# Optimization experiments

Measured on AMD Instinct MI355X. Metric: run time of the kernel, lower is better.

## Reference

```python
import jax, jax.numpy as jnp
import numpy as np

CANVAS = 28
MARGIN = 2
HALF = CANVAS / 2.0          # 14
SCALE = CANVAS / 2.0 - MARGIN  # 12
P = 2        # num_paths
SEG = 4      # final segments
T = 8        # curve samples per bezier segment
AA = 2       # 2x2 = 4 anti-alias subsamples per pixel


def _lin(x, w, b):
    return x @ w + b


def _render(cp, widths, alphas):
    """diffvg-style rasterizer.
    cp: [B,P,S,4,2] cubic bezier control points, widths/alphas: [B,P].
    Returns [B,1,H,W] image over white background (paths paint dark).
    """
    B = cp.shape[0]
    t = jnp.linspace(0.0, 1.0, T)
    mt = 1.0 - t
    basis = jnp.stack([mt**3, 3*mt**2*t, 3*mt*t**2, t**3], axis=1)  # [T,4]
    pts = jnp.einsum('tk,bpskd->bpstd', basis, cp)                   # [B,P,S,T,2]
    q = pts.reshape(B, P, SEG * T, 2)                                # polyline [B,P,M,2]

    # 2x2 subpixel sample grid over the canvas
    Nf = CANVAS * AA
    c = (jnp.arange(Nf, dtype=jnp.float32) + 0.5) / AA               # fine coords
    sy, sx = jnp.meshgrid(c, c, indexing='ij')
    s = jnp.stack([sx.ravel(), sy.ravel()], axis=-1)                 # [Ns,2] (x,y)

    # stroke coverage: distance from each sample to nearest curve sample
    qq = jnp.sum(q * q, axis=-1)                                     # [B,P,M]
    ss = jnp.sum(s * s, axis=-1)                                     # [Ns]
    cr = jnp.einsum('bpmd,nd->bpmn', q, s)                           # [B,P,M,Ns]
    d2 = jnp.maximum(qq[..., None] + ss - 2.0 * cr, 0.0)
    dist = jnp.sqrt(jnp.min(d2, axis=2))                             # [B,P,Ns]
    stroke = jnp.clip(widths[..., None] * 0.5 + 0.5 - dist, 0.0, 1.0)

    # fill coverage: even-odd crossing number on the closed polyline
    qn = jnp.roll(q, -1, axis=2)
    x0, y0 = q[..., 0], q[..., 1]
    x1, y1 = qn[..., 0], qn[..., 1]
    syf, sxf = s[:, 1], s[:, 0]
    crossing_band = (y0[..., None] > syf) != (y1[..., None] > syf)   # [B,P,M,Ns]
    te = (syf - y0[..., None]) / (y1[..., None] - y0[..., None] + 1e-8)
    xint = x0[..., None] + te * (x1 - x0)[..., None]
    ncross = jnp.sum((crossing_band & (sxf < xint)).astype(jnp.int32), axis=2)
    inside = (ncross % 2).astype(dist.dtype)                         # [B,P,Ns]

    cov = jnp.maximum(inside, stroke)
    img = jnp.prod(1.0 - alphas[..., None] * cov, axis=1)            # composite over paths, bg=1
    img = img.reshape(B, CANVAS, AA, CANVAS, AA).mean(axis=(2, 4))   # AA resolve
    return img[:, None]                                              # [B,1,H,W]


def setup_inputs() -> dict:
    key = jax.random.key(0)
    ks = jax.random.split(key, 16)
    def W(k, i, o):
        return jax.random.normal(k, (i, o), jnp.float32) / np.sqrt(i).astype(np.float32)
    B = 128
    return {
        'x': jax.random.uniform(ks[0], (B, 1, 28, 28), jnp.float32),
        'eps': jax.random.normal(ks[1], (B, 64), jnp.float32),
        'enc_w1': W(ks[2], 784, 256), 'enc_b1': jnp.zeros((256,), jnp.float32),
        'enc_w2': W(ks[3], 256, 256), 'enc_b2': jnp.zeros((256,), jnp.float32),
        'mu_w': W(ks[4], 256, 64), 'mu_b': jnp.zeros((64,), jnp.float32),
        'lv_w': W(ks[5], 256, 64), 'lv_b': jnp.zeros((64,), jnp.float32),
        'dec_w1': W(ks[6], 64, 512), 'dec_b1': jnp.zeros((512,), jnp.float32),
        'dec_w2': W(ks[7], 512, 512), 'dec_b2': jnp.zeros((512,), jnp.float32),
        'cp_w': W(ks[8], 512, 28), 'cp_b': jnp.zeros((28,), jnp.float32),
        'ref_w1': W(ks[9], 92, 512), 'ref_b1': jnp.zeros((512,), jnp.float32),
        'ref_w2': W(ks[10], 512, 52), 'ref_b2': jnp.zeros((52,), jnp.float32),
        'wd_w': W(ks[11], 512, 2), 'wd_b': jnp.zeros((2,), jnp.float32),
        'al_w': W(ks[12], 512, 2), 'al_b': jnp.zeros((2,), jnp.float32),
    }


def reference(x, eps, enc_w1, enc_b1, enc_w2, enc_b2, mu_w, mu_b, lv_w, lv_b,
              dec_w1, dec_b1, dec_w2, dec_b2, cp_w, cp_b,
              ref_w1, ref_b1, ref_w2, ref_b2, wd_w, wd_b, al_w, al_b):
    B = x.shape[0]
    # encoder
    h = jax.nn.leaky_relu(_lin(x.reshape(B, -1), enc_w1, enc_b1), 0.2)
    h = jax.nn.leaky_relu(_lin(h, enc_w2, enc_b2), 0.2)
    mu = _lin(h, mu_w, mu_b)
    logvar = _lin(h, lv_w, lv_b)
    z = mu + eps * jnp.exp(0.5 * logvar)
    # hierarchical decoder
    h2 = jax.nn.selu(_lin(jax.nn.selu(_lin(z, dec_w1, dec_b1)), dec_w2, dec_b2))
    coarse = jnp.tanh(_lin(h2, cp_w, cp_b)).reshape(B, P, 7, 2) * SCALE + HALF
    pts_norm = (coarse - HALF) / SCALE
    h_in = jnp.concatenate([z, pts_norm.reshape(B, -1)], axis=-1)
    refined = jnp.tanh(_lin(jax.nn.selu(_lin(h_in, ref_w1, ref_b1)), ref_w2, ref_b2))
    points = refined.reshape(B, P, 13, 2) * SCALE + HALF
    seg_idx = 3 * jnp.arange(SEG)[:, None] + jnp.arange(4)[None, :]  # [S,4]
    control_points = points[:, :, seg_idx, :]                         # [B,P,S,4,2]
    widths = jax.nn.sigmoid(_lin(h2, wd_w, wd_b)) * 2.0 + 1.0
    alphas = jax.nn.sigmoid(_lin(h2, al_w, al_b))
    rendered = 1.0 - _render(control_points, widths, alphas)          # white digit on black
    return (rendered, mu, logvar, control_points, widths, alphas)
```

## Files before the change

### kernel.cpp

```cpp
#include <hip/hip_runtime.h>
#include <math.h>


#define O_MU  100352
#define O_LV  108544
#define O_CP  116736
#define O_WD  124928
#define O_AL  125184

__device__ __forceinline__ float leaky(float x) {
    return x >= 0.0f ? x : 0.2f * x;
}
__device__ __forceinline__ float selu(float x) {
    const float scale = 1.0507009873554805f;
    const float alpha = 1.6732632423543772f;
    return x > 0.0f ? scale * x : scale * (alpha * expm1f(x));
}

__global__ __launch_bounds__(512)
void pipeline(const float* __restrict__ x, const float* __restrict__ eps,
              const float* __restrict__ enc_w1, const float* __restrict__ enc_b1,
              const float* __restrict__ enc_w2, const float* __restrict__ enc_b2,
              const float* __restrict__ mu_w, const float* __restrict__ mu_b,
              const float* __restrict__ lv_w, const float* __restrict__ lv_b,
              const float* __restrict__ dec_w1, const float* __restrict__ dec_b1,
              const float* __restrict__ dec_w2, const float* __restrict__ dec_b2,
              const float* __restrict__ cp_w, const float* __restrict__ cp_b,
              const float* __restrict__ ref_w1, const float* __restrict__ ref_b1,
              const float* __restrict__ ref_w2, const float* __restrict__ ref_b2,
              const float* __restrict__ wd_w, const float* __restrict__ wd_b,
              const float* __restrict__ al_w, const float* __restrict__ al_b,
              float* __restrict__ out) {
    __shared__ float sX[784];
    __shared__ float sPart[512];
    __shared__ float sH1[256];
    __shared__ float sHe[256];
    __shared__ float sML[128];
    __shared__ float sIn[96];
    __shared__ float sD1[512];
    __shared__ float sH2[512];
    __shared__ float sR1[512];
    __shared__ float sP[56];
    __shared__ float sQ[128];
    __shared__ float sWA[4];

    const int row = blockIdx.x;
    const int tid = threadIdx.x;

    for (int i = tid; i < 784; i += 512) sX[i] = x[row * 784 + i];
    __syncthreads();

    {
        const int j = tid & 255, g = tid >> 8;
        const int k0 = g * 392;
        float a0 = 0.f, a1 = 0.f, a2 = 0.f, a3 = 0.f;
        for (int i = 0; i < 392; i += 4) {
            a0 = fmaf(sX[k0 + i + 0], enc_w1[(k0 + i + 0) * 256 + j], a0);
            a1 = fmaf(sX[k0 + i + 1], enc_w1[(k0 + i + 1) * 256 + j], a1);
            a2 = fmaf(sX[k0 + i + 2], enc_w1[(k0 + i + 2) * 256 + j], a2);
            a3 = fmaf(sX[k0 + i + 3], enc_w1[(k0 + i + 3) * 256 + j], a3);
        }
        sPart[tid] = (a0 + a1) + (a2 + a3);
    }
    __syncthreads();
    if (tid < 256) sH1[tid] = leaky(enc_b1[tid] + sPart[tid] + sPart[256 + tid]);
    __syncthreads();

    {
        const int j = tid & 255, g = tid >> 8;
        const int k0 = g * 128;
        float a0 = 0.f, a1 = 0.f, a2 = 0.f, a3 = 0.f;
        for (int i = 0; i < 128; i += 4) {
            a0 = fmaf(sH1[k0 + i + 0], enc_w2[(k0 + i + 0) * 256 + j], a0);
            a1 = fmaf(sH1[k0 + i + 1], enc_w2[(k0 + i + 1) * 256 + j], a1);
            a2 = fmaf(sH1[k0 + i + 2], enc_w2[(k0 + i + 2) * 256 + j], a2);
            a3 = fmaf(sH1[k0 + i + 3], enc_w2[(k0 + i + 3) * 256 + j], a3);
        }
        sPart[tid] = (a0 + a1) + (a2 + a3);
    }
    __syncthreads();
    if (tid < 256) sHe[tid] = leaky(enc_b2[tid] + sPart[tid] + sPart[256 + tid]);
    __syncthreads();

    {
        const int o = tid >> 2, g = tid & 3;
        const int j = o & 63;
        const bool is_lv = o >= 64;
        const float* __restrict__ W = is_lv ? lv_w : mu_w;
        float acc = 0.f;
        for (int k = g; k < 256; k += 4) acc = fmaf(sHe[k], W[k * 64 + j], acc);
        acc += __shfl_xor(acc, 1);
        acc += __shfl_xor(acc, 2);
        if (g == 0) {
            acc += is_lv ? lv_b[j] : mu_b[j];
            out[(is_lv ? O_LV : O_MU) + row * 64 + j] = acc;
            sML[o] = acc;
        }
    }
    __syncthreads();
    if (tid < 64)
        sIn[tid] = fmaf(eps[row * 64 + tid], expf(0.5f * sML[64 + tid]), sML[tid]);
    __syncthreads();

    {
        float acc = dec_b1[tid];
        for (int k = 0; k < 64; k++) acc = fmaf(sIn[k], dec_w1[k * 512 + tid], acc);
        sD1[tid] = selu(acc);
    }
    __syncthreads();

    {
        float a0 = dec_b2[tid], a1 = 0.f, a2 = 0.f, a3 = 0.f;
        for (int k = 0; k < 512; k += 4) {
            a0 = fmaf(sD1[k + 0], dec_w2[(k + 0) * 512 + tid], a0);
            a1 = fmaf(sD1[k + 1], dec_w2[(k + 1) * 512 + tid], a1);
            a2 = fmaf(sD1[k + 2], dec_w2[(k + 2) * 512 + tid], a2);
            a3 = fmaf(sD1[k + 3], dec_w2[(k + 3) * 512 + tid], a3);
        }
        sH2[tid] = selu((a0 + a1) + (a2 + a3));
    }
    __syncthreads();

    {
        const int o = tid >> 4, g = tid & 15;
        const float* __restrict__ W;
        int ldw, col;
        if (o < 28)      { W = cp_w; ldw = 28; col = o; }
        else if (o < 30) { W = wd_w; ldw = 2;  col = o - 28; }
        else             { W = al_w; ldw = 2;  col = o - 30; }
        float acc = 0.f;
        for (int k = g; k < 512; k += 16) acc = fmaf(sH2[k], W[k * ldw + col], acc);
        acc += __shfl_xor(acc, 1);
        acc += __shfl_xor(acc, 2);
        acc += __shfl_xor(acc, 4);
        acc += __shfl_xor(acc, 8);
        if (g == 0) {
            if (o < 28) {
                sIn[64 + o] = tanhf(acc + cp_b[col]);
            } else if (o < 30) {
                float v = 1.f / (1.f + expf(-(acc + wd_b[col])));
                v = fmaf(v, 2.f, 1.f);
                out[O_WD + row * 2 + col] = v;
                sWA[col] = v;
            } else {
                float v = 1.f / (1.f + expf(-(acc + al_b[col])));
                out[O_AL + row * 2 + col] = v;
                sWA[2 + col] = v;
            }
        }
    }
    __syncthreads();

    {
        float acc = ref_b1[tid];
        for (int k = 0; k < 92; k++) acc = fmaf(sIn[k], ref_w1[k * 512 + tid], acc);
        sR1[tid] = selu(acc);
    }
    __syncthreads();

    {
        const int o = tid >> 3, g = tid & 7;
        float acc = 0.f;
        if (o < 52)
            for (int k = g; k < 512; k += 8) acc = fmaf(sR1[k], ref_w2[k * 52 + o], acc);
        acc += __shfl_xor(acc, 1);
        acc += __shfl_xor(acc, 2);
        acc += __shfl_xor(acc, 4);
        if (g == 0 && o < 52)
            sP[o] = fmaf(tanhf(acc + ref_b2[o]), 12.f, 14.f);
    }
    __syncthreads();

    if (tid < 64) {
        int idx = tid;
        int p = idx >> 5, rest = idx & 31;
        int s = rest >> 3, kk = (rest >> 1) & 3, d = idx & 1;
        out[O_CP + row * 64 + idx] = sP[p * 26 + (3 * s + kk) * 2 + d];
    }
    if (tid < 128) {
        int idx = tid;
        int p = idx >> 6, s = (idx >> 4) & 3, ti = (idx >> 1) & 7, d = idx & 1;
        float t = (float)ti / 7.0f;
        float mt = 1.0f - t;
        float c0 = mt * mt * mt;
        float c1 = 3.f * mt * mt * t;
        float c2 = 3.f * mt * t * t;
        float c3 = t * t * t;
        const float* base = sP + p * 26 + (3 * s) * 2 + d;
        sQ[idx] = c0 * base[0] + c1 * base[2] + c2 * base[4] + c3 * base[6];
    }
    __syncthreads();

    const float2* __restrict__ sQ2 = (const float2*)sQ;
    for (int u = tid; u < 3136; u += 512) {
        const int pixel = u >> 2;
        const int sub = u & 3;
        const int py = pixel / 28;
        const int px = pixel - py * 28;
        const float sy = ((float)(2 * py + (sub >> 1)) + 0.5f) * 0.5f;
        const float sx = ((float)(2 * px + (sub & 1)) + 0.5f) * 0.5f;
        float img = 1.0f;
#pragma unroll
        for (int p = 0; p < 2; p++) {
            float dmin2 = 1e30f;
            int cnt = 0;
            float2 cur = sQ2[p * 32];
            bool bp = cur.y > sy;
#pragma unroll
            for (int m = 0; m < 32; m++) {
                float2 nxt = sQ2[p * 32 + ((m + 1) & 31)];
                float dx = sx - cur.x;
                float dy = sy - cur.y;
                dmin2 = fminf(dmin2, fmaf(dx, dx, dy * dy));
                bool bn = nxt.y > sy;
                float den = nxt.y - cur.y + 1e-8f;
                float lhs = dx * den;
                float rhs = dy * (nxt.x - cur.x);
                if ((bp != bn) && ((lhs < rhs) == (den > 0.0f))) cnt++;
                cur = nxt;
                bp = bn;
            }
            float dist = sqrtf(dmin2);
            float stroke = fminf(fmaxf(fmaf(sWA[p], 0.5f, 0.5f) - dist, 0.f), 1.f);
            float cov = fmaxf((float)(cnt & 1), stroke);
            img *= fmaf(-sWA[2 + p], cov, 1.0f);
        }
        img += __shfl_xor(img, 1);
        img += __shfl_xor(img, 2);
        if (sub == 0) out[row * 784 + pixel] = 1.0f - 0.25f * img;
    }
}

extern "C" void kernel_launch(void* const* d_in, const int* in_sizes, int n_in,
                              void* d_out, int out_size, void* d_ws, size_t ws_size,
                              hipStream_t stream) {
    const float* x      = (const float*)d_in[0];
    const float* eps    = (const float*)d_in[1];
    const float* enc_w1 = (const float*)d_in[2];
    const float* enc_b1 = (const float*)d_in[3];
    const float* enc_w2 = (const float*)d_in[4];
    const float* enc_b2 = (const float*)d_in[5];
    const float* mu_w   = (const float*)d_in[6];
    const float* mu_b   = (const float*)d_in[7];
    const float* lv_w   = (const float*)d_in[8];
    const float* lv_b   = (const float*)d_in[9];
    const float* dec_w1 = (const float*)d_in[10];
    const float* dec_b1 = (const float*)d_in[11];
    const float* dec_w2 = (const float*)d_in[12];
    const float* dec_b2 = (const float*)d_in[13];
    const float* cp_w   = (const float*)d_in[14];
    const float* cp_b   = (const float*)d_in[15];
    const float* ref_w1 = (const float*)d_in[16];
    const float* ref_b1 = (const float*)d_in[17];
    const float* ref_w2 = (const float*)d_in[18];
    const float* ref_b2 = (const float*)d_in[19];
    const float* wd_w   = (const float*)d_in[20];
    const float* wd_b   = (const float*)d_in[21];
    const float* al_w   = (const float*)d_in[22];
    const float* al_b   = (const float*)d_in[23];

    float* out = (float*)d_out;

    pipeline<<<128, 512, 0, stream>>>(x, eps, enc_w1, enc_b1, enc_w2, enc_b2,
                                      mu_w, mu_b, lv_w, lv_b, dec_w1, dec_b1,
                                      dec_w2, dec_b2, cp_w, cp_b, ref_w1, ref_b1,
                                      ref_w2, ref_b2, wd_w, wd_b, al_w, al_b,
                                      out);
}
```

Baseline: 232.9 us.

## Double block size and vectorize dense layers with float4 split-K partial sums

Launches 1024 threads per block instead of 512 and rewrites the dense layers so each thread computes four output columns via float4 weight loads over a slice of the reduction dimension. Partial sums go to a shared float4 buffer and are reduced by a subset of threads. The aim is more memory-level parallelism and wider loads on the latency-bound per-row MLP. The cost is extra shared-memory reduction steps, idle threads during the reductions, and higher register pressure at the 1024-thread launch bound.

```diff
diff --git a/kernel.cpp b/kernel.cpp
--- a/kernel.cpp
+++ b/kernel.cpp
@@ -16,8 +16,17 @@
     const float alpha = 1.6732632423543772f;
     return x > 0.0f ? scale * x : scale * (alpha * expm1f(x));
 }
-
-__global__ __launch_bounds__(512)
+__device__ __forceinline__ void fma4(float4& acc, float a, const float4 w) {
+    acc.x = fmaf(a, w.x, acc.x);
+    acc.y = fmaf(a, w.y, acc.y);
+    acc.z = fmaf(a, w.z, acc.z);
+    acc.w = fmaf(a, w.w, acc.w);
+}
+__device__ __forceinline__ void add4(float4& a, const float4 b) {
+    a.x += b.x; a.y += b.y; a.z += b.z; a.w += b.w;
+}
+
+__global__ __launch_bounds__(1024)
 void pipeline(const float* __restrict__ x, const float* __restrict__ eps,
               const float* __restrict__ enc_w1, const float* __restrict__ enc_b1,
               const float* __restrict__ enc_w2, const float* __restrict__ enc_b2,
@@ -31,66 +40,77 @@
               const float* __restrict__ wd_w, const float* __restrict__ wd_b,
               const float* __restrict__ al_w, const float* __restrict__ al_b,
               float* __restrict__ out) {
-    __shared__ float sX[784];
-    __shared__ float sPart[512];
-    __shared__ float sH1[256];
-    __shared__ float sHe[256];
-    __shared__ float sML[128];
-    __shared__ float sIn[96];
-    __shared__ float sD1[512];
-    __shared__ float sH2[512];
-    __shared__ float sR1[512];
-    __shared__ float sP[56];
-    __shared__ float sQ[128];
-    __shared__ float sWA[4];
+    __shared__ float  sX[784];
+    __shared__ float4 sPart4[1024];
+    __shared__ float  sH1[256];
+    __shared__ float  sHe[256];
+    __shared__ float  sML[128];
+    __shared__ float  sIn[96];
+    __shared__ float  sD1[512];
+    __shared__ float  sH2[512];
+    __shared__ float  sR1[512];
+    __shared__ float  sP[56];
+    __shared__ float  sQ[128];
+    __shared__ float  sWA[4];
 
     const int row = blockIdx.x;
     const int tid = threadIdx.x;
 
-    for (int i = tid; i < 784; i += 512) sX[i] = x[row * 784 + i];
-    __syncthreads();
-
-    {
-        const int j = tid & 255, g = tid >> 8;
-        const int k0 = g * 392;
-        float a0 = 0.f, a1 = 0.f, a2 = 0.f, a3 = 0.f;
-        for (int i = 0; i < 392; i += 4) {
-            a0 = fmaf(sX[k0 + i + 0], enc_w1[(k0 + i + 0) * 256 + j], a0);
-            a1 = fmaf(sX[k0 + i + 1], enc_w1[(k0 + i + 1) * 256 + j], a1);
-            a2 = fmaf(sX[k0 + i + 2], enc_w1[(k0 + i + 2) * 256 + j], a2);
-            a3 = fmaf(sX[k0 + i + 3], enc_w1[(k0 + i + 3) * 256 + j], a3);
-        }
-        sPart[tid] = (a0 + a1) + (a2 + a3);
-    }
-    __syncthreads();
-    if (tid < 256) sH1[tid] = leaky(enc_b1[tid] + sPart[tid] + sPart[256 + tid]);
-    __syncthreads();
-
-    {
-        const int j = tid & 255, g = tid >> 8;
-        const int k0 = g * 128;
-        float a0 = 0.f, a1 = 0.f, a2 = 0.f, a3 = 0.f;
-        for (int i = 0; i < 128; i += 4) {
-            a0 = fmaf(sH1[k0 + i + 0], enc_w2[(k0 + i + 0) * 256 + j], a0);
-            a1 = fmaf(sH1[k0 + i + 1], enc_w2[(k0 + i + 1) * 256 + j], a1);
-            a2 = fmaf(sH1[k0 + i + 2], enc_w2[(k0 + i + 2) * 256 + j], a2);
-            a3 = fmaf(sH1[k0 + i + 3], enc_w2[(k0 + i + 3) * 256 + j], a3);
-        }
-        sPart[tid] = (a0 + a1) + (a2 + a3);
-    }
-    __syncthreads();
-    if (tid < 256) sHe[tid] = leaky(enc_b2[tid] + sPart[tid] + sPart[256 + tid]);
-    __syncthreads();
-
-    {
-        const int o = tid >> 2, g = tid & 3;
+    if (tid < 784) sX[tid] = x[row * 784 + tid];
+    __syncthreads();
+
+    {
+        const int jv = tid & 63, g = tid >> 6;
+        const float4* __restrict__ W4 = (const float4*)enc_w1;
+        const int k0 = g * 49;
+        float4 acc = {0.f, 0.f, 0.f, 0.f};
+#pragma unroll 7
+        for (int i = 0; i < 49; i++) {
+            fma4(acc, sX[k0 + i], W4[(k0 + i) * 64 + jv]);
+        }
+        sPart4[g * 64 + jv] = acc;
+    }
+    __syncthreads();
+    if (tid < 64) {
+        float4 s = ((const float4*)enc_b1)[tid];
+#pragma unroll
+        for (int g = 0; g < 16; g++) add4(s, sPart4[g * 64 + tid]);
+        s.x = leaky(s.x); s.y = leaky(s.y); s.z = leaky(s.z); s.w = leaky(s.w);
+        ((float4*)sH1)[tid] = s;
+    }
+    __syncthreads();
+
+    {
+        const int jv = tid & 63, g = tid >> 6;
+        const float4* __restrict__ W4 = (const float4*)enc_w2;
+        const int k0 = g * 16;
+        float4 acc = {0.f, 0.f, 0.f, 0.f};
+#pragma unroll
+        for (int i = 0; i < 16; i++) {
+            fma4(acc, sH1[k0 + i], W4[(k0 + i) * 64 + jv]);
+        }
+        sPart4[g * 64 + jv] = acc;
+    }
+    __syncthreads();
+    if (tid < 64) {
+        float4 s = ((const float4*)enc_b2)[tid];
+#pragma unroll
+        for (int g = 0; g < 16; g++) add4(s, sPart4[g * 64 + tid]);
+        s.x = leaky(s.x); s.y = leaky(s.y); s.z = leaky(s.z); s.w = leaky(s.w);
+        ((float4*)sHe)[tid] = s;
+    }
+    __syncthreads();
+
+    {
+        const int o = tid >> 3, g = tid & 7;
         const int j = o & 63;
         const bool is_lv = o >= 64;
         const float* __restrict__ W = is_lv ? lv_w : mu_w;
         float acc = 0.f;
-        for (int k = g; k < 256; k += 4) acc = fmaf(sHe[k], W[k * 64 + j], acc);
+        for (int k = g; k < 256; k += 8) acc = fmaf(sHe[k], W[k * 64 + j], acc);
         acc += __shfl_xor(acc, 1);
         acc += __shfl_xor(acc, 2);
+        acc += __shfl_xor(acc, 4);
         if (g == 0) {
             acc += is_lv ? lv_b[j] : mu_b[j];
             out[(is_lv ? O_LV : O_MU) + row * 64 + j] = acc;
@@ -103,37 +123,61 @@
     __syncthreads();
 
     {
-        float acc = dec_b1[tid];
-        for (int k = 0; k < 64; k++) acc = fmaf(sIn[k], dec_w1[k * 512 + tid], acc);
-        sD1[tid] = selu(acc);
-    }
-    __syncthreads();
-
-    {
-        float a0 = dec_b2[tid], a1 = 0.f, a2 = 0.f, a3 = 0.f;
-        for (int k = 0; k < 512; k += 4) {
-            a0 = fmaf(sD1[k + 0], dec_w2[(k + 0) * 512 + tid], a0);
-            a1 = fmaf(sD1[k + 1], dec_w2[(k + 1) * 512 + tid], a1);
-            a2 = fmaf(sD1[k + 2], dec_w2[(k + 2) * 512 + tid], a2);
-            a3 = fmaf(sD1[k + 3], dec_w2[(k + 3) * 512 + tid], a3);
-        }
-        sH2[tid] = selu((a0 + a1) + (a2 + a3));
-    }
-    __syncthreads();
-
-    {
-        const int o = tid >> 4, g = tid & 15;
+        const int jv = tid & 127, g = tid >> 7;
+        const float4* __restrict__ W4 = (const float4*)dec_w1;
+        const int k0 = g * 8;
+        float4 acc = {0.f, 0.f, 0.f, 0.f};
+#pragma unroll
+        for (int i = 0; i < 8; i++) {
+            fma4(acc, sIn[k0 + i], W4[(k0 + i) * 128 + jv]);
+        }
+        sPart4[g * 128 + jv] = acc;
+    }
+    __syncthreads();
+    if (tid < 128) {
+        float4 s = ((const float4*)dec_b1)[tid];
+#pragma unroll
+        for (int g = 0; g < 8; g++) add4(s, sPart4[g * 128 + tid]);
+        s.x = selu(s.x); s.y = selu(s.y); s.z = selu(s.z); s.w = selu(s.w);
+        ((float4*)sD1)[tid] = s;
+    }
+    __syncthreads();
+
+    {
+        const int jv = tid & 127, g = tid >> 7;
+        const float4* __restrict__ W4 = (const float4*)dec_w2;
+        const int k0 = g * 64;
+        float4 acc = {0.f, 0.f, 0.f, 0.f};
+#pragma unroll 8
+        for (int i = 0; i < 64; i++) {
+            fma4(acc, sD1[k0 + i], W4[(k0 + i) * 128 + jv]);
+        }
+        sPart4[g * 128 + jv] = acc;
+    }
+    __syncthreads();
+    if (tid < 128) {
+        float4 s = ((const float4*)dec_b2)[tid];
+#pragma unroll
+        for (int g = 0; g < 8; g++) add4(s, sPart4[g * 128 + tid]);
+        s.x = selu(s.x); s.y = selu(s.y); s.z = selu(s.z); s.w = selu(s.w);
+        ((float4*)sH2)[tid] = s;
+    }
+    __syncthreads();
+
+    {
+        const int o = tid >> 5, g = tid & 31;
         const float* __restrict__ W;
         int ldw, col;
         if (o < 28)      { W = cp_w; ldw = 28; col = o; }
         else if (o < 30) { W = wd_w; ldw = 2;  col = o - 28; }
         else             { W = al_w; ldw = 2;  col = o - 30; }
         float acc = 0.f;
-        for (int k = g; k < 512; k += 16) acc = fmaf(sH2[k], W[k * ldw + col], acc);
+        for (int k = g; k < 512; k += 32) acc = fmaf(sH2[k], W[k * ldw + col], acc);
         acc += __shfl_xor(acc, 1);
         acc += __shfl_xor(acc, 2);
         acc += __shfl_xor(acc, 4);
         acc += __shfl_xor(acc, 8);
+        acc += __shfl_xor(acc, 16);
         if (g == 0) {
             if (o < 28) {
                 sIn[64 + o] = tanhf(acc + cp_b[col]);
@@ -152,20 +196,35 @@
     __syncthreads();
 
     {
-        float acc = ref_b1[tid];
-        for (int k = 0; k < 92; k++) acc = fmaf(sIn[k], ref_w1[k * 512 + tid], acc);
-        sR1[tid] = selu(acc);
-    }
-    __syncthreads();
-
-    {
-        const int o = tid >> 3, g = tid & 7;
+        const int jv = tid & 127, g = tid >> 7;
+        const float4* __restrict__ W4 = (const float4*)ref_w1;
+        const int k0 = g * 12;
+        const int kend = (k0 + 12 < 92) ? (k0 + 12) : 92;
+        float4 acc = {0.f, 0.f, 0.f, 0.f};
+        for (int k = k0; k < kend; k++) {
+            fma4(acc, sIn[k], W4[k * 128 + jv]);
+        }
+        sPart4[g * 128 + jv] = acc;
+    }
+    __syncthreads();
+    if (tid < 128) {
+        float4 s = ((const float4*)ref_b1)[tid];
+#pragma unroll
+        for (int g = 0; g < 8; g++) add4(s, sPart4[g * 128 + tid]);
+        s.x = selu(s.x); s.y = selu(s.y); s.z = selu(s.z); s.w = selu(s.w);
+        ((float4*)sR1)[tid] = s;
+    }
+    __syncthreads();
+
+    {
+        const int o = tid >> 4, g = tid & 15;
         float acc = 0.f;
         if (o < 52)
-            for (int k = g; k < 512; k += 8) acc = fmaf(sR1[k], ref_w2[k * 52 + o], acc);
+            for (int k = g; k < 512; k += 16) acc = fmaf(sR1[k], ref_w2[k * 52 + o], acc);
         acc += __shfl_xor(acc, 1);
         acc += __shfl_xor(acc, 2);
         acc += __shfl_xor(acc, 4);
+        acc += __shfl_xor(acc, 8);
         if (g == 0 && o < 52)
             sP[o] = fmaf(tanhf(acc + ref_b2[o]), 12.f, 14.f);
     }
@@ -192,7 +251,7 @@
     __syncthreads();
 
     const float2* __restrict__ sQ2 = (const float2*)sQ;
-    for (int u = tid; u < 3136; u += 512) {
+    for (int u = tid; u < 3136; u += 1024) {
         const int pixel = u >> 2;
         const int sub = u & 3;
         const int py = pixel / 28;
@@ -261,9 +320,9 @@
 
     float* out = (float*)d_out;
 
-    pipeline<<<128, 512, 0, stream>>>(x, eps, enc_w1, enc_b1, enc_w2, enc_b2,
-                                      mu_w, mu_b, lv_w, lv_b, dec_w1, dec_b1,
-                                      dec_w2, dec_b2, cp_w, cp_b, ref_w1, ref_b1,
-                                      ref_w2, ref_b2, wd_w, wd_b, al_w, al_b,
-                                      out);
-}
+    pipeline<<<128, 1024, 0, stream>>>(x, eps, enc_w1, enc_b1, enc_w2, enc_b2,
+                                       mu_w, mu_b, lv_w, lv_b, dec_w1, dec_b1,
+                                       dec_w2, dec_b2, cp_w, cp_b, ref_w1, ref_b1,
+                                       ref_w2, ref_b2, wd_w, wd_b, al_w, al_b,
+                                       out);
+}
```

After: 294.2 us. 26.3% more time.

## Split each layer across 16-block groups with grid flags and row batching

Applied to the files above, without the earlier changes.

The grid becomes 256 blocks in groups of 16, each group handling 8 batch rows. Within a group, each block computes a column slice of every MLP layer with float4 weight loads, so each weight is fetched once per 8 rows instead of once per row. Blocks exchange activations through a workspace buffer and spin-wait on per-phase flags, and the rasterization is also split across the 16 blocks. The flags are set to 1 and never cleared, so unless the workspace is zeroed before every call, later launches may skip the waits and race. The design also depends on all blocks of a group being resident at the same time.

```diff
diff --git a/kernel.cpp b/kernel.cpp
--- a/kernel.cpp
+++ b/kernel.cpp
@@ -8,6 +8,15 @@
 #define O_WD  124928
 #define O_AL  125184
 
+#define F4_A1   0
+#define F4_A2   8192
+#define F4_MLV  16384
+#define F4_D1   20480
+#define F4_H2   36864
+#define F4_R1   53248
+#define F4_PN   69632
+#define F4_PTS  70656
+
 __device__ __forceinline__ float leaky(float x) {
     return x >= 0.0f ? x : 0.2f * x;
 }
@@ -16,8 +25,36 @@
     const float alpha = 1.6732632423543772f;
     return x > 0.0f ? scale * x : scale * (alpha * expm1f(x));
 }
-
-__global__ __launch_bounds__(512)
+__device__ __forceinline__ void fma4(float4& acc, float a, const float4 w) {
+    acc.x = fmaf(a, w.x, acc.x);
+    acc.y = fmaf(a, w.y, acc.y);
+    acc.z = fmaf(a, w.z, acc.z);
+    acc.w = fmaf(a, w.w, acc.w);
+}
+__device__ __forceinline__ void red4(float4& v, int m) {
+    v.x += __shfl_xor(v.x, m);
+    v.y += __shfl_xor(v.y, m);
+    v.z += __shfl_xor(v.z, m);
+    v.w += __shfl_xor(v.w, m);
+}
+
+__device__ __forceinline__ void gsync(int* flags, int ph, int rg, int ct, int tid) {
+    __syncthreads();
+    __builtin_amdgcn_fence(__ATOMIC_RELEASE, "agent");
+    __syncthreads();
+    if (tid == 0)
+        __hip_atomic_store(&flags[ph * 256 + rg * 16 + ct], 1,
+                           __ATOMIC_RELAXED, __HIP_MEMORY_SCOPE_AGENT);
+    if (tid < 16) {
+        while (__hip_atomic_load(&flags[ph * 256 + rg * 16 + tid],
+                                 __ATOMIC_RELAXED, __HIP_MEMORY_SCOPE_AGENT) != 1)
+            __builtin_amdgcn_s_sleep(1);
+    }
+    __syncthreads();
+    __builtin_amdgcn_fence(__ATOMIC_ACQUIRE, "agent");
+}
+
+__global__ __launch_bounds__(512, 1)
 void pipeline(const float* __restrict__ x, const float* __restrict__ eps,
               const float* __restrict__ enc_w1, const float* __restrict__ enc_b1,
               const float* __restrict__ enc_w2, const float* __restrict__ enc_b2,
@@ -30,175 +67,269 @@
               const float* __restrict__ ref_w2, const float* __restrict__ ref_b2,
               const float* __restrict__ wd_w, const float* __restrict__ wd_b,
               const float* __restrict__ al_w, const float* __restrict__ al_b,
-              float* __restrict__ out) {
-    __shared__ float sX[784];
-    __shared__ float sPart[512];
-    __shared__ float sH1[256];
-    __shared__ float sHe[256];
-    __shared__ float sML[128];
-    __shared__ float sIn[96];
-    __shared__ float sD1[512];
-    __shared__ float sH2[512];
-    __shared__ float sR1[512];
-    __shared__ float sP[56];
-    __shared__ float sQ[128];
-    __shared__ float sWA[4];
-
-    const int row = blockIdx.x;
+              float* __restrict__ out, int* __restrict__ flags,
+              float4* __restrict__ wbuf) {
+    __shared__ float sBig[6272];
+    __shared__ float sIn[8 * 96];
+    __shared__ float sWA[8 * 4];
+    __shared__ float sP[8 * 56];
+    __shared__ float sQ[8 * 128];
+
+    const int b   = blockIdx.x;
+    const int rg  = b >> 4;
+    const int ct  = b & 15;
     const int tid = threadIdx.x;
-
-    for (int i = tid; i < 784; i += 512) sX[i] = x[row * 784 + i];
-    __syncthreads();
-
-    {
-        const int j = tid & 255, g = tid >> 8;
-        const int k0 = g * 392;
-        float a0 = 0.f, a1 = 0.f, a2 = 0.f, a3 = 0.f;
-        for (int i = 0; i < 392; i += 4) {
-            a0 = fmaf(sX[k0 + i + 0], enc_w1[(k0 + i + 0) * 256 + j], a0);
-            a1 = fmaf(sX[k0 + i + 1], enc_w1[(k0 + i + 1) * 256 + j], a1);
-            a2 = fmaf(sX[k0 + i + 2], enc_w1[(k0 + i + 2) * 256 + j], a2);
-            a3 = fmaf(sX[k0 + i + 3], enc_w1[(k0 + i + 3) * 256 + j], a3);
-        }
-        sPart[tid] = (a0 + a1) + (a2 + a3);
-    }
-    __syncthreads();
-    if (tid < 256) sH1[tid] = leaky(enc_b1[tid] + sPart[tid] + sPart[256 + tid]);
-    __syncthreads();
-
-    {
-        const int j = tid & 255, g = tid >> 8;
-        const int k0 = g * 128;
-        float a0 = 0.f, a1 = 0.f, a2 = 0.f, a3 = 0.f;
-        for (int i = 0; i < 128; i += 4) {
-            a0 = fmaf(sH1[k0 + i + 0], enc_w2[(k0 + i + 0) * 256 + j], a0);
-            a1 = fmaf(sH1[k0 + i + 1], enc_w2[(k0 + i + 1) * 256 + j], a1);
-            a2 = fmaf(sH1[k0 + i + 2], enc_w2[(k0 + i + 2) * 256 + j], a2);
-            a3 = fmaf(sH1[k0 + i + 3], enc_w2[(k0 + i + 3) * 256 + j], a3);
-        }
-        sPart[tid] = (a0 + a1) + (a2 + a3);
-    }
-    __syncthreads();
-    if (tid < 256) sHe[tid] = leaky(enc_b2[tid] + sPart[tid] + sPart[256 + tid]);
-    __syncthreads();
-
-    {
-        const int o = tid >> 2, g = tid & 3;
-        const int j = o & 63;
-        const bool is_lv = o >= 64;
-        const float* __restrict__ W = is_lv ? lv_w : mu_w;
-        float acc = 0.f;
-        for (int k = g; k < 256; k += 4) acc = fmaf(sHe[k], W[k * 64 + j], acc);
-        acc += __shfl_xor(acc, 1);
-        acc += __shfl_xor(acc, 2);
-        if (g == 0) {
-            acc += is_lv ? lv_b[j] : mu_b[j];
-            out[(is_lv ? O_LV : O_MU) + row * 64 + j] = acc;
-            sML[o] = acc;
-        }
-    }
-    __syncthreads();
-    if (tid < 64)
-        sIn[tid] = fmaf(eps[row * 64 + tid], expf(0.5f * sML[64 + tid]), sML[tid]);
-    __syncthreads();
-
-    {
-        float acc = dec_b1[tid];
-        for (int k = 0; k < 64; k++) acc = fmaf(sIn[k], dec_w1[k * 512 + tid], acc);
-        sD1[tid] = selu(acc);
-    }
-    __syncthreads();
-
-    {
-        float a0 = dec_b2[tid], a1 = 0.f, a2 = 0.f, a3 = 0.f;
-        for (int k = 0; k < 512; k += 4) {
-            a0 = fmaf(sD1[k + 0], dec_w2[(k + 0) * 512 + tid], a0);
-            a1 = fmaf(sD1[k + 1], dec_w2[(k + 1) * 512 + tid], a1);
-            a2 = fmaf(sD1[k + 2], dec_w2[(k + 2) * 512 + tid], a2);
-            a3 = fmaf(sD1[k + 3], dec_w2[(k + 3) * 512 + tid], a3);
-        }
-        sH2[tid] = selu((a0 + a1) + (a2 + a3));
-    }
-    __syncthreads();
-
-    {
-        const int o = tid >> 4, g = tid & 15;
-        const float* __restrict__ W;
-        int ldw, col;
-        if (o < 28)      { W = cp_w; ldw = 28; col = o; }
-        else if (o < 30) { W = wd_w; ldw = 2;  col = o - 28; }
-        else             { W = al_w; ldw = 2;  col = o - 30; }
-        float acc = 0.f;
-        for (int k = g; k < 512; k += 16) acc = fmaf(sH2[k], W[k * ldw + col], acc);
-        acc += __shfl_xor(acc, 1);
-        acc += __shfl_xor(acc, 2);
-        acc += __shfl_xor(acc, 4);
-        acc += __shfl_xor(acc, 8);
-        if (g == 0) {
-            if (o < 28) {
-                sIn[64 + o] = tanhf(acc + cp_b[col]);
-            } else if (o < 30) {
-                float v = 1.f / (1.f + expf(-(acc + wd_b[col])));
-                v = fmaf(v, 2.f, 1.f);
-                out[O_WD + row * 2 + col] = v;
-                sWA[col] = v;
+    const int w   = tid >> 6;
+    const int l   = tid & 63;
+    const int row = rg * 8 + w;
+
+    for (int i = tid; i < 6272; i += 512) sBig[i] = x[rg * 6272 + i];
+    __syncthreads();
+
+    {
+        const int jc = l & 3, gi = l >> 2;
+        const float4* __restrict__ W4 = (const float4*)enc_w1;
+        const float* __restrict__ A = sBig + w * 784;
+        const int base = ct * 4 + jc;
+        const int k0 = gi * 49;
+        float4 acc = {0, 0, 0, 0};
+        for (int i = 0; i < 49; i++)
+            fma4(acc, A[k0 + i], W4[(k0 + i) * 64 + base]);
+        red4(acc, 4); red4(acc, 8); red4(acc, 16); red4(acc, 32);
+        if (gi == 0) {
+            float4 s = ((const float4*)enc_b1)[base];
+            s.x = leaky(s.x + acc.x); s.y = leaky(s.y + acc.y);
+            s.z = leaky(s.z + acc.z); s.w = leaky(s.w + acc.w);
+            wbuf[F4_A1 + row * 64 + base] = s;
+        }
+    }
+    gsync(flags, 0, rg, ct, tid);
+    ((float4*)sBig)[tid] = wbuf[F4_A1 + (rg * 8 + (tid >> 6)) * 64 + (tid & 63)];
+    __syncthreads();
+
+    {
+        const int jc = l & 3, gi = l >> 2;
+        const float4* __restrict__ W4 = (const float4*)enc_w2;
+        const float* __restrict__ A = sBig + w * 256;
+        const int base = ct * 4 + jc;
+        const int k0 = gi * 16;
+        float4 acc = {0, 0, 0, 0};
+        for (int i = 0; i < 16; i++)
+            fma4(acc, A[k0 + i], W4[(k0 + i) * 64 + base]);
+        red4(acc, 4); red4(acc, 8); red4(acc, 16); red4(acc, 32);
+        if (gi == 0) {
+            float4 s = ((const float4*)enc_b2)[base];
+            s.x = leaky(s.x + acc.x); s.y = leaky(s.y + acc.y);
+            s.z = leaky(s.z + acc.z); s.w = leaky(s.w + acc.w);
+            wbuf[F4_A2 + row * 64 + base] = s;
+        }
+    }
+    gsync(flags, 1, rg, ct, tid);
+    ((float4*)sBig)[tid] = wbuf[F4_A2 + (rg * 8 + (tid >> 6)) * 64 + (tid & 63)];
+    __syncthreads();
+
+    {
+        const int jc = l & 1, gi = l >> 1;
+        const bool is_lv = ct >= 8;
+        const float4* __restrict__ W4 = (const float4*)(is_lv ? lv_w : mu_w);
+        const float* __restrict__ A = sBig + w * 256;
+        const int base = (ct & 7) * 2 + jc;
+        const int k0 = gi * 8;
+        float4 acc = {0, 0, 0, 0};
+        for (int i = 0; i < 8; i++)
+            fma4(acc, A[k0 + i], W4[(k0 + i) * 16 + base]);
+        red4(acc, 2); red4(acc, 4); red4(acc, 8); red4(acc, 16); red4(acc, 32);
+        if (gi == 0) {
+            float4 s = is_lv ? ((const float4*)lv_b)[base] : ((const float4*)mu_b)[base];
+            s.x += acc.x; s.y += acc.y; s.z += acc.z; s.w += acc.w;
+            ((float4*)(out + (is_lv ? O_LV : O_MU)))[row * 16 + base] = s;
+            wbuf[F4_MLV + row * 32 + (is_lv ? 16 : 0) + base] = s;
+        }
+    }
+    gsync(flags, 2, rg, ct, tid);
+    if (tid < 256)
+        ((float4*)sBig)[tid] = wbuf[F4_MLV + (rg * 8 + (tid >> 5)) * 32 + (tid & 31)];
+    __syncthreads();
+    {
+        const int rr = tid >> 6, j = tid & 63;
+        float mu = sBig[rr * 128 + j];
+        float lv = sBig[rr * 128 + 64 + j];
+        sIn[rr * 96 + j] = fmaf(eps[(rg * 8 + rr) * 64 + j], expf(0.5f * lv), mu);
+    }
+    __syncthreads();
+
+    {
+        const int jc = l & 7, gi = l >> 3;
+        const float4* __restrict__ W4 = (const float4*)dec_w1;
+        const float* __restrict__ A = sIn + w * 96;
+        const int base = ct * 8 + jc;
+        const int k0 = gi * 8;
+        float4 acc = {0, 0, 0, 0};
+        for (int i = 0; i < 8; i++)
+            fma4(acc, A[k0 + i], W4[(k0 + i) * 128 + base]);
+        red4(acc, 8); red4(acc, 16); red4(acc, 32);
+        if (gi == 0) {
+            float4 s = ((const float4*)dec_b1)[base];
+            s.x = selu(s.x + acc.x); s.y = selu(s.y + acc.y);
+            s.z = selu(s.z + acc.z); s.w = selu(s.w + acc.w);
+            wbuf[F4_D1 + row * 128 + base] = s;
+        }
+    }
+    gsync(flags, 3, rg, ct, tid);
+    ((float4*)sBig)[tid]       = wbuf[F4_D1 + (rg * 8 + (tid >> 7)) * 128 + (tid & 127)];
+    ((float4*)sBig)[tid + 512] = wbuf[F4_D1 + (rg * 8 + ((tid + 512) >> 7)) * 128 + (tid & 127)];
+    __syncthreads();
+
+    {
+        const int jc = l & 7, gi = l >> 3;
+        const float4* __restrict__ W4 = (const float4*)dec_w2;
+        const float* __restrict__ A = sBig + w * 512;
+        const int base = ct * 8 + jc;
+        const int k0 = gi * 64;
+        float4 acc = {0, 0, 0, 0};
+        for (int i = 0; i < 64; i++)
+            fma4(acc, A[k0 + i], W4[(k0 + i) * 128 + base]);
+        red4(acc, 8); red4(acc, 16); red4(acc, 32);
+        if (gi == 0) {
+            float4 s = ((const float4*)dec_b2)[base];
+            s.x = selu(s.x + acc.x); s.y = selu(s.y + acc.y);
+            s.z = selu(s.z + acc.z); s.w = selu(s.w + acc.w);
+            wbuf[F4_H2 + row * 128 + base] = s;
+        }
+    }
+    gsync(flags, 4, rg, ct, tid);
+    ((float4*)sBig)[tid]       = wbuf[F4_H2 + (rg * 8 + (tid >> 7)) * 128 + (tid & 127)];
+    ((float4*)sBig)[tid + 512] = wbuf[F4_H2 + (rg * 8 + ((tid + 512) >> 7)) * 128 + (tid & 127)];
+    __syncthreads();
+
+    {
+        const float* __restrict__ A = sBig + w * 512;
+        const float* w0p; const float* w1p; int str;
+        if (ct < 14)      { w0p = cp_w + 2 * ct; w1p = cp_w + 2 * ct + 1; str = 28; }
+        else if (ct == 14){ w0p = wd_w;          w1p = wd_w + 1;          str = 2; }
+        else              { w0p = al_w;          w1p = al_w + 1;          str = 2; }
+        float a0 = 0.f, a1v = 0.f;
+        for (int i = 0; i < 8; i++) {
+            int k = l + 64 * i;
+            float av = A[k];
+            a0  = fmaf(av, w0p[k * str], a0);
+            a1v = fmaf(av, w1p[k * str], a1v);
+        }
+        for (int m = 1; m <= 32; m <<= 1) {
+            a0 += __shfl_xor(a0, m);
+            a1v += __shfl_xor(a1v, m);
+        }
+        if (l == 0) {
+            float* wpn = (float*)(wbuf + F4_PN);
+            if (ct < 14) {
+                wpn[row * 32 + 2 * ct]     = tanhf(a0 + cp_b[2 * ct]);
+                wpn[row * 32 + 2 * ct + 1] = tanhf(a1v + cp_b[2 * ct + 1]);
+            } else if (ct == 14) {
+                float v0 = fmaf(1.f / (1.f + expf(-(a0 + wd_b[0]))), 2.f, 1.f);
+                float v1 = fmaf(1.f / (1.f + expf(-(a1v + wd_b[1]))), 2.f, 1.f);
+                out[O_WD + row * 2 + 0] = v0; out[O_WD + row * 2 + 1] = v1;
+                wpn[row * 32 + 28] = v0; wpn[row * 32 + 29] = v1;
             } else {
-                float v = 1.f / (1.f + expf(-(acc + al_b[col])));
-                out[O_AL + row * 2 + col] = v;
-                sWA[2 + col] = v;
+                float v0 = 1.f / (1.f + expf(-(a0 + al_b[0])));
+                float v1 = 1.f / (1.f + expf(-(a1v + al_b[1])));
+                out[O_AL + row * 2 + 0] = v0; out[O_AL + row * 2 + 1] = v1;
+                wpn[row * 32 + 30] = v0; wpn[row * 32 + 31] = v1;
             }
         }
     }
-    __syncthreads();
-
-    {
-        float acc = ref_b1[tid];
-        for (int k = 0; k < 92; k++) acc = fmaf(sIn[k], ref_w1[k * 512 + tid], acc);
-        sR1[tid] = selu(acc);
-    }
-    __syncthreads();
-
-    {
-        const int o = tid >> 3, g = tid & 7;
-        float acc = 0.f;
-        if (o < 52)
-            for (int k = g; k < 512; k += 8) acc = fmaf(sR1[k], ref_w2[k * 52 + o], acc);
-        acc += __shfl_xor(acc, 1);
-        acc += __shfl_xor(acc, 2);
-        acc += __shfl_xor(acc, 4);
-        if (g == 0 && o < 52)
-            sP[o] = fmaf(tanhf(acc + ref_b2[o]), 12.f, 14.f);
-    }
-    __syncthreads();
-
-    if (tid < 64) {
-        int idx = tid;
-        int p = idx >> 5, rest = idx & 31;
-        int s = rest >> 3, kk = (rest >> 1) & 3, d = idx & 1;
-        out[O_CP + row * 64 + idx] = sP[p * 26 + (3 * s + kk) * 2 + d];
-    }
-    if (tid < 128) {
-        int idx = tid;
-        int p = idx >> 6, s = (idx >> 4) & 3, ti = (idx >> 1) & 7, d = idx & 1;
+    gsync(flags, 5, rg, ct, tid);
+    if (tid < 256) {
+        const float* wpn = (const float*)(wbuf + F4_PN);
+        const int rr = tid >> 5, i = tid & 31;
+        float v = wpn[(rg * 8 + rr) * 32 + i];
+        if (i < 28) sIn[rr * 96 + 64 + i] = v;
+        else        sWA[rr * 4 + (i - 28)] = v;
+    }
+    __syncthreads();
+
+    {
+        const int jc = l & 7, gi = l >> 3;
+        const float4* __restrict__ W4 = (const float4*)ref_w1;
+        const float* __restrict__ A = sIn + w * 96;
+        const int base = ct * 8 + jc;
+        const int k0 = (92 * gi) >> 3, k1 = (92 * (gi + 1)) >> 3;
+        float4 acc = {0, 0, 0, 0};
+        for (int k = k0; k < k1; k++)
+            fma4(acc, A[k], W4[k * 128 + base]);
+        red4(acc, 8); red4(acc, 16); red4(acc, 32);
+        if (gi == 0) {
+            float4 s = ((const float4*)ref_b1)[base];
+            s.x = selu(s.x + acc.x); s.y = selu(s.y + acc.y);
+            s.z = selu(s.z + acc.z); s.w = selu(s.w + acc.w);
+            wbuf[F4_R1 + row * 128 + base] = s;
+        }
+    }
+    gsync(flags, 6, rg, ct, tid);
+    ((float4*)sBig)[tid]       = wbuf[F4_R1 + (rg * 8 + (tid >> 7)) * 128 + (tid & 127)];
+    ((float4*)sBig)[tid + 512] = wbuf[F4_R1 + (rg * 8 + ((tid + 512) >> 7)) * 128 + (tid & 127)];
+    __syncthreads();
+
+    if (ct < 13) {
+        const float* __restrict__ A = sBig + w * 512;
+        const int o0 = ct * 4;
+        float4 acc = {0, 0, 0, 0};
+        for (int i = 0; i < 8; i++) {
+            int k = l + 64 * i;
+            float av = A[k];
+            const float* Wk = ref_w2 + k * 52 + o0;
+            acc.x = fmaf(av, Wk[0], acc.x);
+            acc.y = fmaf(av, Wk[1], acc.y);
+            acc.z = fmaf(av, Wk[2], acc.z);
+            acc.w = fmaf(av, Wk[3], acc.w);
+        }
+        red4(acc, 1); red4(acc, 2); red4(acc, 4);
+        red4(acc, 8); red4(acc, 16); red4(acc, 32);
+        if (l == 0) {
+            float4 p;
+            p.x = fmaf(tanhf(acc.x + ref_b2[o0 + 0]), 12.f, 14.f);
+            p.y = fmaf(tanhf(acc.y + ref_b2[o0 + 1]), 12.f, 14.f);
+            p.z = fmaf(tanhf(acc.z + ref_b2[o0 + 2]), 12.f, 14.f);
+            p.w = fmaf(tanhf(acc.w + ref_b2[o0 + 3]), 12.f, 14.f);
+            wbuf[F4_PTS + row * 13 + ct] = p;
+        }
+    }
+    gsync(flags, 7, rg, ct, tid);
+    if (tid < 104) {
+        const int rr = tid / 13, c = tid - rr * 13;
+        *((float4*)(sP + rr * 56 + c * 4)) = wbuf[F4_PTS + (rg * 8 + rr) * 13 + c];
+    }
+    __syncthreads();
+
+    if (ct < 8 && tid < 64) {
+        const int idx = tid;
+        const int p = idx >> 5, rest = idx & 31;
+        const int s = rest >> 3, kk = (rest >> 1) & 3, d = idx & 1;
+        out[O_CP + (rg * 8 + ct) * 64 + idx] = sP[ct * 56 + p * 26 + (3 * s + kk) * 2 + d];
+    }
+    for (int idx = tid; idx < 1024; idx += 512) {
+        const int rr = idx >> 7, i = idx & 127;
+        const int p = i >> 6, s = (i >> 4) & 3, ti = (i >> 1) & 7, d = i & 1;
         float t = (float)ti / 7.0f;
         float mt = 1.0f - t;
         float c0 = mt * mt * mt;
         float c1 = 3.f * mt * mt * t;
         float c2 = 3.f * mt * t * t;
         float c3 = t * t * t;
-        const float* base = sP + p * 26 + (3 * s) * 2 + d;
-        sQ[idx] = c0 * base[0] + c1 * base[2] + c2 * base[4] + c3 * base[6];
-    }
-    __syncthreads();
-
-    const float2* __restrict__ sQ2 = (const float2*)sQ;
-    for (int u = tid; u < 3136; u += 512) {
+        const float* base = sP + rr * 56 + p * 26 + (3 * s) * 2 + d;
+        sQ[rr * 128 + i] = c0 * base[0] + c1 * base[2] + c2 * base[4] + c3 * base[6];
+    }
+    __syncthreads();
+
+    for (int it = tid; it < 1568; it += 512) {
+        const int rr = it / 196;
+        const int u = ct * 196 + (it - rr * 196);
         const int pixel = u >> 2;
         const int sub = u & 3;
         const int py = pixel / 28;
         const int px = pixel - py * 28;
         const float sy = ((float)(2 * py + (sub >> 1)) + 0.5f) * 0.5f;
         const float sx = ((float)(2 * px + (sub & 1)) + 0.5f) * 0.5f;
+        const float2* __restrict__ sQ2 = (const float2*)(sQ + rr * 128);
         float img = 1.0f;
 #pragma unroll
         for (int p = 0; p < 2; p++) {
@@ -221,13 +352,13 @@
                 bp = bn;
             }
             float dist = sqrtf(dmin2);
-            float stroke = fminf(fmaxf(fmaf(sWA[p], 0.5f, 0.5f) - dist, 0.f), 1.f);
+            float stroke = fminf(fmaxf(fmaf(sWA[rr * 4 + p], 0.5f, 0.5f) - dist, 0.f), 1.f);
             float cov = fmaxf((float)(cnt & 1), stroke);
-            img *= fmaf(-sWA[2 + p], cov, 1.0f);
+            img *= fmaf(-sWA[rr * 4 + 2 + p], cov, 1.0f);
         }
         img += __shfl_xor(img, 1);
         img += __shfl_xor(img, 2);
-        if (sub == 0) out[row * 784 + pixel] = 1.0f - 0.25f * img;
+        if (sub == 0) out[(rg * 8 + rr) * 784 + pixel] = 1.0f - 0.25f * img;
     }
 }
 
@@ -259,11 +390,13 @@
     const float* al_w   = (const float*)d_in[22];
     const float* al_b   = (const float*)d_in[23];
 
-    float* out = (float*)d_out;
-
-    pipeline<<<128, 512, 0, stream>>>(x, eps, enc_w1, enc_b1, enc_w2, enc_b2,
+    float* out   = (float*)d_out;
+    int*   flags = (int*)d_ws;
+    float4* wbuf = (float4*)((char*)d_ws + 8192);
+
+    pipeline<<<256, 512, 0, stream>>>(x, eps, enc_w1, enc_b1, enc_w2, enc_b2,
                                       mu_w, mu_b, lv_w, lv_b, dec_w1, dec_b1,
                                       dec_w2, dec_b2, cp_w, cp_b, ref_w1, ref_b1,
                                       ref_w2, ref_b2, wd_w, wd_b, al_w, al_b,
-                                      out);
-}
+                                      out, flags, wbuf);
+}
```

Measured after the change: 403.3 us. +73.2%, slower.
